# Performance work log

Measured on AMD Instinct MI355X. Metric: run time of the kernel, lower is better.

Reference implementation:

```python
import jax, jax.numpy as jnp
import numpy as np
from jax import lax


def setup_inputs() -> dict:
    key = jax.random.key(0)
    k1, k2 = jax.random.split(key)
    B, C_out, C_in, K, H, W = 16, 128, 128, 3, 64, 64
    features = jax.random.normal(k1, (B, C_in, H, W), dtype=jnp.float32)
    dynamic_kernel = jax.random.normal(k2, (B, C_out, C_in, K, K), dtype=jnp.float32)
    return {"features": features, "dynamic_kernel": dynamic_kernel}


def reference(features, dynamic_kernel):
    # Per-sample dynamic conv. unfold+bmm in torch == cross-correlation (conv2d)
    # with the per-sample kernel; we express it as a vmapped implicit-GEMM conv
    # instead of materializing the (C_in*K*K, H*W) unfold buffer.
    padding = 1

    def conv_one(x, w):  # x: (C_in, H, W), w: (C_out, C_in, K, K)
        return lax.conv_general_dilated(
            x[None],                      # (1, C_in, H, W)
            w,
            window_strides=(1, 1),
            padding=[(padding, padding), (padding, padding)],
            dimension_numbers=("NCHW", "OIHW", "NCHW"),
        )[0]                              # (C_out, H, W)

    return jax.vmap(conv_one)(features, dynamic_kernel)  # (B, C_out, H, W)
```

## Files before the change

kernel.cpp:

```cpp
#include <hip/hip_runtime.h>
#include <stdint.h>

#define BATCH 16
#define CIN   128
#define COUT  128
#define IMG_H 64
#define IMG_W 64
#define HW    4096
#define KTOT  1152
#define XH    66
#define XW    66
#define BM    128
#define BN    128
#define BK    64
#define NSTEPS 18
#define ASTEP 8192

typedef __attribute__((ext_vector_type(8))) __bf16 bf16x8;
typedef __attribute__((ext_vector_type(4))) float  f32x4;
typedef __attribute__((address_space(1))) const void* gas_p;
typedef __attribute__((address_space(3))) void*       las_p;

static __device__ __forceinline__ unsigned short f2bf(float f) {
  union { float f; uint32_t u; } c; c.f = f;
  uint32_t r = c.u + 0x7fffu + ((c.u >> 16) & 1u);
  return (unsigned short)(r >> 16);
}

static __device__ __forceinline__ void gload_lds16(const unsigned short* g, unsigned short* l) {
  __builtin_amdgcn_global_load_lds((gas_p)g, (las_p)l, 16, 0, 0);
}

__global__ void prep_w(const float* __restrict__ w, unsigned short* __restrict__ wt4) {
  const int b    = blockIdx.x / NSTEPS;
  const int step = blockIdx.x % NSTEPS;
  const int khkw = step >> 1;
  const int cib  = (step & 1) << 6;
  const float* wb = w + (size_t)b * COUT * KTOT;
  unsigned short* dst = wt4 + ((size_t)b * NSTEPS + step) * ASTEP;
#pragma unroll
  for (int i = 0; i < 4; ++i) {
    const int c  = i * 256 + threadIdx.x;
    const int cq = c >> 7;
    const int co = c & 127;
    const int ci0 = cib + cq * 8;
    const float* src = wb + (size_t)co * KTOT + (size_t)ci0 * 9 + khkw;
    uint32_t p[4];
#pragma unroll
    for (int e = 0; e < 4; ++e)
      p[e] = (uint32_t)f2bf(src[(2 * e) * 9]) | ((uint32_t)f2bf(src[(2 * e + 1) * 9]) << 16);
    *(uint4*)&dst[(size_t)c * 8] = make_uint4(p[0], p[1], p[2], p[3]);
  }
}

__global__ void prep_x(const float* __restrict__ x, unsigned short* __restrict__ xpad) {
  __shared__ uint32_t tile[64 * 68];
  const int t = threadIdx.x;
  const int b = blockIdx.x >> 6;
  const int h = blockIdx.x & 63;
  const float* xb = x + (size_t)b * CIN * HW + h * IMG_W;
  uint32_t* xpw = (uint32_t*)xpad;

  const int lane16 = t & 15;
  const int g      = t >> 4;
#pragma unroll
  for (int it = 0; it < 4; ++it) {
    const int ci = it * 32 + g * 2;
    const float4 va = *(const float4*)(xb + (size_t)ci * HW + lane16 * 4);
    const float4 vb = *(const float4*)(xb + (size_t)(ci + 1) * HW + lane16 * 4);
    const float av[4] = {va.x, va.y, va.z, va.w};
    const float bv[4] = {vb.x, vb.y, vb.z, vb.w};
#pragma unroll
    for (int cc = 0; cc < 4; ++cc)
      tile[(lane16 * 4 + cc) * 68 + it * 16 + g] =
          (uint32_t)f2bf(av[cc]) | ((uint32_t)f2bf(bv[cc]) << 16);
  }
  __syncthreads();

  const uint32_t base_w = (((uint32_t)b * XH + h + 1) * XW + 1) * 64;
#pragma unroll
  for (int it = 0; it < 4; ++it) {
    const int o = it * 256 + t;
    const uint4 v = *(const uint4*)&tile[(o >> 4) * 68 + (o & 15) * 4];
    *(uint4*)&xpw[base_w + o * 4] = v;
  }
  if (t < 128) {
    const uint32_t row_w = ((uint32_t)b * XH + h + 1) * XW * 64;
    const int col = (t >> 6) ? 65 : 0;
    xpw[row_w + col * 64 + (t & 63)] = 0u;
  }
  if (h == 0) {
    const uint32_t r0  = (uint32_t)b * XH * XW * 64;
    const uint32_t r65 = ((uint32_t)b * XH + 65) * XW * 64;
    for (int i = t; i < XW * 64; i += 256) { xpw[r0 + i] = 0u; xpw[r65 + i] = 0u; }
  }
}

__global__ __launch_bounds__(256, 2) void dynconv_gemm(
    const unsigned short* __restrict__ wt4,
    const unsigned short* __restrict__ xpad,
    float* __restrict__ out) {
  __shared__ alignas(16) unsigned short As[ASTEP];
  __shared__ alignas(16) unsigned short Bs[ASTEP];

  const int t    = threadIdx.x;
  const int b    = blockIdx.y;
  const int pix0 = blockIdx.x * BN;
  const int oh0  = pix0 >> 6;

  const int lane = t & 63;
  const int wave = t >> 6;
  const int wm   = (wave & 1) << 6;
  const int wn   = (wave >> 1) << 6;
  const int l15  = lane & 15;
  const int quad = lane >> 4;

  const unsigned short* abase = wt4 + (size_t)b * NSTEPS * ASTEP + (size_t)t * 8;
  const unsigned short* xb    = xpad + (size_t)b * XH * XW * CIN;

  const unsigned short* bbase[4];
#pragma unroll
  for (int i = 0; i < 4; ++i) {
    const int c   = i * 256 + t;
    const int cq  = c >> 7;
    const int pix = c & 127;
    bbase[i] = xb + (size_t)((oh0 + (pix >> 6)) * XW + (pix & 63)) * CIN + cq * 8;
  }

  unsigned short* alds[4];
  unsigned short* blds[4];
#pragma unroll
  for (int i = 0; i < 4; ++i) {
    alds[i] = &As[(i * 256 + wave * 64) * 8];
    blds[i] = &Bs[(i * 256 + wave * 64) * 8];
  }

  f32x4 acc[4][4] = {};

  for (int step = 0; step < NSTEPS; ++step) {
    const int khkw = step >> 1;
    const int kh   = (khkw * 11) >> 5;
    const int kw   = khkw - kh * 3;
    const int boff = (kh * XW + kw) * CIN + ((step & 1) << 6);
    const unsigned short* astep = abase + (size_t)step * ASTEP;

#pragma unroll
    for (int i = 0; i < 4; ++i) gload_lds16(astep + i * 256 * 8, alds[i]);
#pragma unroll
    for (int i = 0; i < 4; ++i) gload_lds16(bbase[i] + boff, blds[i]);
    __syncthreads();

#pragma unroll
    for (int ks = 0; ks < 2; ++ks) {
      const int cqb = (ks * 4 + quad) * 128;
      bf16x8 af[4], bf[4];
#pragma unroll
      for (int i = 0; i < 4; ++i) af[i] = *(const bf16x8*)&As[(cqb + wm + i * 16 + l15) * 8];
#pragma unroll
      for (int j = 0; j < 4; ++j) bf[j] = *(const bf16x8*)&Bs[(cqb + wn + j * 16 + l15) * 8];
#pragma unroll
      for (int i = 0; i < 4; ++i)
#pragma unroll
        for (int j = 0; j < 4; ++j)
          acc[i][j] = __builtin_amdgcn_mfma_f32_16x16x32_bf16(af[i], bf[j], acc[i][j], 0, 0, 0);
    }
    __syncthreads();
  }

  float* obase = out + (size_t)b * COUT * HW + pix0;
#pragma unroll
  for (int i = 0; i < 4; ++i) {
#pragma unroll
    for (int r = 0; r < 4; ++r) {
      const int row = wm + i * 16 + quad * 4 + r;
      float* orow = obase + (size_t)row * HW;
#pragma unroll
      for (int j = 0; j < 4; ++j)
        orow[wn + j * 16 + l15] = acc[i][j][r];
    }
  }
}

__global__ void dynconv_naive(const float* __restrict__ x, const float* __restrict__ w,
                              float* __restrict__ out) {
  const int o   = blockIdx.x * 256 + threadIdx.x;
  const int pix = o & (HW - 1);
  const int co  = (o >> 12) & (COUT - 1);
  const int b   = o >> 19;
  const int oh  = pix >> 6, ow = pix & 63;
  const float* xb = x + (size_t)b * CIN * HW;
  const float* wb = w + ((size_t)b * COUT + co) * CIN * 9;
  float s = 0.f;
  for (int ci = 0; ci < CIN; ++ci) {
    const float* xc = xb + ci * HW;
    const float* wc = wb + ci * 9;
#pragma unroll
    for (int kh = 0; kh < 3; ++kh) {
      const int ih = oh + kh - 1;
      if ((unsigned)ih >= IMG_H) continue;
#pragma unroll
      for (int kw = 0; kw < 3; ++kw) {
        const int iw = ow + kw - 1;
        if ((unsigned)iw >= IMG_W) continue;
        s += xc[ih * IMG_W + iw] * wc[kh * 3 + kw];
      }
    }
  }
  out[o] = s;
}

extern "C" void kernel_launch(void* const* d_in, const int* in_sizes, int n_in,
                              void* d_out, int out_size, void* d_ws, size_t ws_size,
                              hipStream_t stream) {
  const float* x = (const float*)d_in[0];
  const float* w = (const float*)d_in[1];
  float* out = (float*)d_out;

  const size_t wt_bytes = (size_t)BATCH * NSTEPS * ASTEP * sizeof(unsigned short);
  const size_t xp_bytes = (size_t)BATCH * XH * XW * CIN * sizeof(unsigned short);

  if (ws_size >= wt_bytes + xp_bytes) {
    unsigned short* wt4  = (unsigned short*)d_ws;
    unsigned short* xpad = (unsigned short*)((char*)d_ws + wt_bytes);
    prep_w<<<BATCH * NSTEPS, 256, 0, stream>>>(w, wt4);
    prep_x<<<BATCH * IMG_H, 256, 0, stream>>>(x, xpad);
    dim3 grid(HW / BN, BATCH);
    dynconv_gemm<<<grid, 256, 0, stream>>>(wt4, xpad, out);
  } else {
    dynconv_naive<<<(BATCH * COUT * HW) / 256, 256, 0, stream>>>(x, w, out);
  }
}
```

Measured before the change: 132.7 us.

## Halve GEMM pixel tile, re-layout padded input by channel groups, fuse prep kernels

The two preprocessing kernels are merged into one launch that branches on block index. The padded input moves from pixel-major/channel-minor to a row × channel-group × column layout, so each 64-pixel row tile for one 8-channel group is contiguous. The GEMM tile shrinks from 128 to 64 pixels, one output row per block, which doubles the grid to 1024 blocks and raises launch_bounds occupancy to 4. In exchange, each block reloads the full weight tile for half as much work, so weight reads per output double and arithmetic intensity drops.

```diff
diff --git a/kernel.cpp b/kernel.cpp
--- a/kernel.cpp
+++ b/kernel.cpp
@@ -10,11 +10,13 @@
 #define KTOT  1152
 #define XH    66
 #define XW    66
+#define NCQ   16
 #define BM    128
-#define BN    128
+#define BN    64
 #define BK    64
 #define NSTEPS 18
 #define ASTEP 8192
+#define BSTEP 4096
 
 typedef __attribute__((ext_vector_type(8))) __bf16 bf16x8;
 typedef __attribute__((ext_vector_type(4))) float  f32x4;
@@ -31,143 +33,143 @@
   __builtin_amdgcn_global_load_lds((gas_p)g, (las_p)l, 16, 0, 0);
 }
 
-__global__ void prep_w(const float* __restrict__ w, unsigned short* __restrict__ wt4) {
-  const int b    = blockIdx.x / NSTEPS;
-  const int step = blockIdx.x % NSTEPS;
-  const int khkw = step >> 1;
-  const int cib  = (step & 1) << 6;
-  const float* wb = w + (size_t)b * COUT * KTOT;
-  unsigned short* dst = wt4 + ((size_t)b * NSTEPS + step) * ASTEP;
-#pragma unroll
-  for (int i = 0; i < 4; ++i) {
-    const int c  = i * 256 + threadIdx.x;
-    const int cq = c >> 7;
-    const int co = c & 127;
-    const int ci0 = cib + cq * 8;
-    const float* src = wb + (size_t)co * KTOT + (size_t)ci0 * 9 + khkw;
-    uint32_t p[4];
-#pragma unroll
-    for (int e = 0; e < 4; ++e)
-      p[e] = (uint32_t)f2bf(src[(2 * e) * 9]) | ((uint32_t)f2bf(src[(2 * e + 1) * 9]) << 16);
-    *(uint4*)&dst[(size_t)c * 8] = make_uint4(p[0], p[1], p[2], p[3]);
-  }
-}
-
-__global__ void prep_x(const float* __restrict__ x, unsigned short* __restrict__ xpad) {
-  __shared__ uint32_t tile[64 * 68];
+__global__ void prep_fused(const float* __restrict__ x, const float* __restrict__ w,
+                           unsigned short* __restrict__ wt4, unsigned short* __restrict__ xpad) {
   const int t = threadIdx.x;
-  const int b = blockIdx.x >> 6;
-  const int h = blockIdx.x & 63;
-  const float* xb = x + (size_t)b * CIN * HW + h * IMG_W;
-  uint32_t* xpw = (uint32_t*)xpad;
-
-  const int lane16 = t & 15;
-  const int g      = t >> 4;
-#pragma unroll
-  for (int it = 0; it < 4; ++it) {
-    const int ci = it * 32 + g * 2;
-    const float4 va = *(const float4*)(xb + (size_t)ci * HW + lane16 * 4);
-    const float4 vb = *(const float4*)(xb + (size_t)(ci + 1) * HW + lane16 * 4);
-    const float av[4] = {va.x, va.y, va.z, va.w};
-    const float bv[4] = {vb.x, vb.y, vb.z, vb.w};
-#pragma unroll
-    for (int cc = 0; cc < 4; ++cc)
-      tile[(lane16 * 4 + cc) * 68 + it * 16 + g] =
-          (uint32_t)f2bf(av[cc]) | ((uint32_t)f2bf(bv[cc]) << 16);
-  }
-  __syncthreads();
-
-  const uint32_t base_w = (((uint32_t)b * XH + h + 1) * XW + 1) * 64;
-#pragma unroll
-  for (int it = 0; it < 4; ++it) {
-    const int o = it * 256 + t;
-    const uint4 v = *(const uint4*)&tile[(o >> 4) * 68 + (o & 15) * 4];
-    *(uint4*)&xpw[base_w + o * 4] = v;
-  }
-  if (t < 128) {
-    const uint32_t row_w = ((uint32_t)b * XH + h + 1) * XW * 64;
-    const int col = (t >> 6) ? 65 : 0;
-    xpw[row_w + col * 64 + (t & 63)] = 0u;
-  }
-  if (h == 0) {
-    const uint32_t r0  = (uint32_t)b * XH * XW * 64;
-    const uint32_t r65 = ((uint32_t)b * XH + 65) * XW * 64;
-    for (int i = t; i < XW * 64; i += 256) { xpw[r0 + i] = 0u; xpw[r65 + i] = 0u; }
-  }
-}
-
-__global__ __launch_bounds__(256, 2) void dynconv_gemm(
+  if (blockIdx.x < BATCH * IMG_H) {
+    __shared__ uint32_t tile[64 * 68];
+    const int b = blockIdx.x >> 6;
+    const int h = blockIdx.x & 63;
+    const float* xb = x + (size_t)b * CIN * HW + h * IMG_W;
+    uint4* xp4 = (uint4*)xpad;
+
+    const int lane16 = t & 15;
+    const int g      = t >> 4;
+#pragma unroll
+    for (int it = 0; it < 4; ++it) {
+      const int ci = it * 32 + g * 2;
+      const float4 va = *(const float4*)(xb + (size_t)ci * HW + lane16 * 4);
+      const float4 vb = *(const float4*)(xb + (size_t)(ci + 1) * HW + lane16 * 4);
+      const float av[4] = {va.x, va.y, va.z, va.w};
+      const float bv[4] = {vb.x, vb.y, vb.z, vb.w};
+#pragma unroll
+      for (int cc = 0; cc < 4; ++cc)
+        tile[(lane16 * 4 + cc) * 68 + it * 16 + g] =
+            (uint32_t)f2bf(av[cc]) | ((uint32_t)f2bf(bv[cc]) << 16);
+    }
+    __syncthreads();
+
+    const uint32_t rbase = ((uint32_t)b * XH + h + 1) * NCQ;
+#pragma unroll
+    for (int it = 0; it < 4; ++it) {
+      const int o   = it * 256 + t;
+      const int cqg = o >> 6;
+      const int wc  = o & 63;
+      const uint4 v = *(const uint4*)&tile[wc * 68 + cqg * 4];
+      xp4[(rbase + cqg) * XW + wc + 1] = v;
+    }
+    if (t < 32) {
+      const int cqg = t & 15;
+      const int col = (t >> 4) ? 65 : 0;
+      xp4[(rbase + cqg) * XW + col] = make_uint4(0, 0, 0, 0);
+    }
+    if (h == 0) {
+      const uint32_t r0  = (uint32_t)b * XH * NCQ * XW;
+      const uint32_t r65 = ((uint32_t)b * XH + 65) * NCQ * XW;
+      for (int i = t; i < NCQ * XW; i += 256) {
+        xp4[r0 + i]  = make_uint4(0, 0, 0, 0);
+        xp4[r65 + i] = make_uint4(0, 0, 0, 0);
+      }
+    }
+  } else {
+    const int idx  = blockIdx.x - BATCH * IMG_H;
+    const int b    = idx / NSTEPS;
+    const int step = idx % NSTEPS;
+    const int khkw = step >> 1;
+    const int cib  = (step & 1) << 6;
+    const float* wb = w + (size_t)b * COUT * KTOT;
+    unsigned short* dst = wt4 + ((size_t)b * NSTEPS + step) * ASTEP;
+#pragma unroll
+    for (int i = 0; i < 4; ++i) {
+      const int c  = i * 256 + t;
+      const int cq = c >> 7;
+      const int co = c & 127;
+      const int ci0 = cib + cq * 8;
+      const float* src = wb + (size_t)co * KTOT + (size_t)ci0 * 9 + khkw;
+      uint32_t p[4];
+#pragma unroll
+      for (int e = 0; e < 4; ++e)
+        p[e] = (uint32_t)f2bf(src[(2 * e) * 9]) | ((uint32_t)f2bf(src[(2 * e + 1) * 9]) << 16);
+      *(uint4*)&dst[(size_t)c * 8] = make_uint4(p[0], p[1], p[2], p[3]);
+    }
+  }
+}
+
+__global__ __launch_bounds__(256, 4) void dynconv_gemm(
     const unsigned short* __restrict__ wt4,
     const unsigned short* __restrict__ xpad,
     float* __restrict__ out) {
   __shared__ alignas(16) unsigned short As[ASTEP];
-  __shared__ alignas(16) unsigned short Bs[ASTEP];
+  __shared__ alignas(16) unsigned short Bs[BSTEP];
 
   const int t    = threadIdx.x;
   const int b    = blockIdx.y;
-  const int pix0 = blockIdx.x * BN;
-  const int oh0  = pix0 >> 6;
+  const int oh   = blockIdx.x;
 
   const int lane = t & 63;
   const int wave = t >> 6;
   const int wm   = (wave & 1) << 6;
-  const int wn   = (wave >> 1) << 6;
+  const int wn   = (wave >> 1) << 5;
   const int l15  = lane & 15;
   const int quad = lane >> 4;
 
   const unsigned short* abase = wt4 + (size_t)b * NSTEPS * ASTEP + (size_t)t * 8;
-  const unsigned short* xb    = xpad + (size_t)b * XH * XW * CIN;
-
-  const unsigned short* bbase[4];
-#pragma unroll
-  for (int i = 0; i < 4; ++i) {
-    const int c   = i * 256 + t;
-    const int cq  = c >> 7;
-    const int pix = c & 127;
-    bbase[i] = xb + (size_t)((oh0 + (pix >> 6)) * XW + (pix & 63)) * CIN + cq * 8;
-  }
+  const unsigned short* xb = xpad + (size_t)b * XH * NCQ * XW * 8;
+  const unsigned short* bbase[2];
+#pragma unroll
+  for (int i = 0; i < 2; ++i)
+    bbase[i] = xb + (size_t)(((i * 4 + wave) * XW) + lane) * 8;
 
   unsigned short* alds[4];
-  unsigned short* blds[4];
-#pragma unroll
-  for (int i = 0; i < 4; ++i) {
-    alds[i] = &As[(i * 256 + wave * 64) * 8];
-    blds[i] = &Bs[(i * 256 + wave * 64) * 8];
-  }
-
-  f32x4 acc[4][4] = {};
+  unsigned short* blds[2];
+#pragma unroll
+  for (int i = 0; i < 4; ++i) alds[i] = &As[(i * 256 + wave * 64) * 8];
+#pragma unroll
+  for (int i = 0; i < 2; ++i) blds[i] = &Bs[((i * 4 + wave) * 64) * 8];
+
+  f32x4 acc[4][2] = {};
 
   for (int step = 0; step < NSTEPS; ++step) {
     const int khkw = step >> 1;
     const int kh   = (khkw * 11) >> 5;
     const int kw   = khkw - kh * 3;
-    const int boff = (kh * XW + kw) * CIN + ((step & 1) << 6);
+    const size_t boff = ((size_t)((oh + kh) * NCQ + ((step & 1) << 3)) * XW + kw) * 8;
     const unsigned short* astep = abase + (size_t)step * ASTEP;
 
 #pragma unroll
-    for (int i = 0; i < 4; ++i) gload_lds16(astep + i * 256 * 8, alds[i]);
-#pragma unroll
-    for (int i = 0; i < 4; ++i) gload_lds16(bbase[i] + boff, blds[i]);
+    for (int i = 0; i < 4; ++i) gload_lds16(astep + i * 2048, alds[i]);
+#pragma unroll
+    for (int i = 0; i < 2; ++i) gload_lds16(bbase[i] + boff, blds[i]);
     __syncthreads();
 
 #pragma unroll
     for (int ks = 0; ks < 2; ++ks) {
-      const int cqb = (ks * 4 + quad) * 128;
-      bf16x8 af[4], bf[4];
-#pragma unroll
-      for (int i = 0; i < 4; ++i) af[i] = *(const bf16x8*)&As[(cqb + wm + i * 16 + l15) * 8];
-#pragma unroll
-      for (int j = 0; j < 4; ++j) bf[j] = *(const bf16x8*)&Bs[(cqb + wn + j * 16 + l15) * 8];
+      const int cq = ks * 4 + quad;
+      bf16x8 af[4], bf[2];
+#pragma unroll
+      for (int i = 0; i < 4; ++i) af[i] = *(const bf16x8*)&As[(cq * 128 + wm + i * 16 + l15) * 8];
+#pragma unroll
+      for (int j = 0; j < 2; ++j) bf[j] = *(const bf16x8*)&Bs[(cq * 64 + wn + j * 16 + l15) * 8];
 #pragma unroll
       for (int i = 0; i < 4; ++i)
 #pragma unroll
-        for (int j = 0; j < 4; ++j)
+        for (int j = 0; j < 2; ++j)
           acc[i][j] = __builtin_amdgcn_mfma_f32_16x16x32_bf16(af[i], bf[j], acc[i][j], 0, 0, 0);
     }
     __syncthreads();
   }
 
-  float* obase = out + (size_t)b * COUT * HW + pix0;
+  float* obase = out + (size_t)b * COUT * HW + oh * 64;
 #pragma unroll
   for (int i = 0; i < 4; ++i) {
 #pragma unroll
@@ -175,7 +177,7 @@
       const int row = wm + i * 16 + quad * 4 + r;
       float* orow = obase + (size_t)row * HW;
 #pragma unroll
-      for (int j = 0; j < 4; ++j)
+      for (int j = 0; j < 2; ++j)
         orow[wn + j * 16 + l15] = acc[i][j][r];
     }
   }
@@ -217,14 +219,13 @@
   float* out = (float*)d_out;
 
   const size_t wt_bytes = (size_t)BATCH * NSTEPS * ASTEP * sizeof(unsigned short);
-  const size_t xp_bytes = (size_t)BATCH * XH * XW * CIN * sizeof(unsigned short);
+  const size_t xp_bytes = (size_t)BATCH * XH * NCQ * XW * 8 * sizeof(unsigned short);
 
   if (ws_size >= wt_bytes + xp_bytes) {
     unsigned short* wt4  = (unsigned short*)d_ws;
     unsigned short* xpad = (unsigned short*)((char*)d_ws + wt_bytes);
-    prep_w<<<BATCH * NSTEPS, 256, 0, stream>>>(w, wt4);
-    prep_x<<<BATCH * IMG_H, 256, 0, stream>>>(x, xpad);
-    dim3 grid(HW / BN, BATCH);
+    prep_fused<<<BATCH * IMG_H + BATCH * NSTEPS, 256, 0, stream>>>(x, w, wt4, xpad);
+    dim3 grid(IMG_H, BATCH);
     dynconv_gemm<<<grid, 256, 0, stream>>>(wt4, xpad, out);
   } else {
     dynconv_naive<<<(BATCH * COUT * HW) / 256, 256, 0, stream>>>(x, w, out);
```

Result: faster. 122.4 us (-7.7%).
